# Kernel optimization log

Hardware: AMD Instinct MI355X
Metric: run time of the kernel (lower is better)

The kernel has to match this reference:

```python
import jax, jax.numpy as jnp
import numpy as np

B, S, D = 2, 2048, 1024
H = 16
HD = D // H
SCALE = float(np.sqrt(HD))


def setup_inputs() -> dict:
    key = jax.random.key(0)
    ks = jax.random.split(key, 10)
    def lin(k):
        # xavier_uniform for [out, in] = [D, D]
        bound = float(np.sqrt(6.0 / (D + D)))
        return jax.random.uniform(k, (D, D), jnp.float32, -bound, bound)
    return {
        "hidden_states": jax.random.normal(ks[0], (B, S, D), jnp.float32),
        "attention_mask": jnp.ones((B, S), jnp.float32),
        "Wq": lin(ks[1]), "bq": jnp.zeros((D,), jnp.float32),
        "Wk": lin(ks[2]), "bk": jnp.zeros((D,), jnp.float32),
        "Wv": lin(ks[3]), "bv": jnp.zeros((D,), jnp.float32),
        "Wo": lin(ks[4]), "bo": jnp.zeros((D,), jnp.float32),
    }


def _heads(x):
    # [B,S,D] -> [B,H,S,HD]
    return x.reshape(B, S, H, HD).transpose(0, 2, 1, 3)


def secure_softmax(scores):
    c = jnp.clip(scores, -3.0, 3.0)
    sig = 0.5 + 0.25 * c - 0.01 * c ** 3
    sig = jnp.clip(sig, 0.01, 0.99)
    return sig / (jnp.sum(sig, axis=-1, keepdims=True) + 1e-8)


def reference(hidden_states, attention_mask, Wq, bq, Wk, bk, Wv, bv, Wo, bo):
    q = _heads(hidden_states @ Wq.T + bq)
    k = _heads(hidden_states @ Wk.T + bk)
    v = _heads(hidden_states @ Wv.T + bv)
    # [B,H,S,S]
    scores = jnp.einsum("bhqd,bhkd->bhqk", q, k) / SCALE
    scores = scores + (1.0 - attention_mask[:, None, None, :]) * -10000.0
    probs = secure_softmax(scores)
    ctx = jnp.einsum("bhqk,bhkd->bhqd", probs, v)
    ctx = ctx.transpose(0, 2, 1, 3).reshape(B, S, D)
    return ctx @ Wo.T + bo
```

## Files before the change

### kernel.cpp

```cpp
#include <hip/hip_runtime.h>
#include <stdint.h>

#define B_ 2
#define S_ 2048
#define D_ 1024
#define H_ 16
#define HD_ 64
#define M_ (B_*S_)

typedef __bf16 bf16;
typedef __attribute__((ext_vector_type(8))) __bf16 bf16x8;
typedef __attribute__((ext_vector_type(4))) float f32x4;

__device__ __forceinline__ void gload16(const bf16* g, bf16* l) {
    __builtin_amdgcn_global_load_lds(
        (const __attribute__((address_space(1))) void*)g,
        (__attribute__((address_space(3))) void*)l, 16, 0, 0);
}

__global__ void k_cvt_all(const float* __restrict__ hs,
                          const float* __restrict__ Wq, const float* __restrict__ Wk,
                          const float* __restrict__ Wv, const float* __restrict__ Wo,
                          bf16* __restrict__ hb,
                          bf16* __restrict__ wqb, bf16* __restrict__ wkb,
                          bf16* __restrict__ wvb, bf16* __restrict__ wob) {
    int blk = blockIdx.x;
    const float* s; bf16* d; int base;
    if (blk < 2048) { s = hs; d = hb; base = blk; }
    else {
        int r = blk - 2048; int which = r >> 9; base = r & 511;
        s = (which==0)?Wq:(which==1)?Wk:(which==2)?Wv:Wo;
        d = (which==0)?wqb:(which==1)?wkb:(which==2)?wvb:wob;
    }
    int idx = base*2048 + threadIdx.x*8;
    float4 a = *(const float4*)(s + idx);
    float4 b = *(const float4*)(s + idx + 4);
    bf16 o[8] = {(bf16)a.x,(bf16)a.y,(bf16)a.z,(bf16)a.w,
                 (bf16)b.x,(bf16)b.y,(bf16)b.z,(bf16)b.w};
    *(int4*)(d + idx) = *(const int4*)o;
}

__global__ __launch_bounds__(256) void k_gemm_qkv(
    const bf16* __restrict__ X,
    const bf16* __restrict__ Wq, const bf16* __restrict__ Wk, const bf16* __restrict__ Wv,
    const float* __restrict__ bq, const float* __restrict__ bk, const float* __restrict__ bv,
    bf16* __restrict__ Qo, bf16* __restrict__ Ko, bf16* __restrict__ Vo)
{
    const int z = blockIdx.z;
    const bf16* W = (z==0) ? Wq : (z==1) ? Wk : Wv;
    const float* bias = (z==0) ? bq : (z==1) ? bk : bv;
    const int n0 = blockIdx.x * 128;
    const int m0 = blockIdx.y * 128;
    const int t = threadIdx.x;
    const int w = t >> 6, lane = t & 63, quad = lane >> 4, l15 = lane & 15;
    const int lr = lane >> 3;
    const int lc = (lane & 7) ^ lr;
    const int sx = l15 & 7;
    const int mw = (w >> 1) * 64, nw = (w & 1) * 64;

    __shared__ __align__(16) char smraw[128*136*2];
    bf16* As  = (bf16*)smraw;
    bf16* Bs  = (bf16*)(smraw + 16384);
    bf16* epi = (bf16*)smraw;

    f32x4 acc[4][4];
    #pragma unroll
    for (int i = 0; i < 4; i++)
        #pragma unroll
        for (int j = 0; j < 4; j++)
            acc[i][j] = (f32x4){0.f,0.f,0.f,0.f};

    const bf16* gA = X + (size_t)(m0 + w*8 + lr)*D_ + lc*8;
    const bf16* gB = W + (size_t)(n0 + w*8 + lr)*D_ + lc*8;

    for (int k0 = 0; k0 < D_; k0 += 64) {
        #pragma unroll
        for (int c = 0; c < 4; c++) {
            gload16(gA + (size_t)c*32*D_ + k0, &As[c*2048 + w*512]);
            gload16(gB + (size_t)c*32*D_ + k0, &Bs[c*2048 + w*512]);
        }
        __syncthreads();
        #pragma unroll
        for (int ks = 0; ks < 2; ks++) {
            bf16x8 af[4], bfr[4];
            #pragma unroll
            for (int i = 0; i < 4; i++)
                af[i] = *(const bf16x8*)&As[(mw + i*16 + l15)*64 + (((ks*4+quad)^sx)*8)];
            #pragma unroll
            for (int j = 0; j < 4; j++)
                bfr[j] = *(const bf16x8*)&Bs[(nw + j*16 + l15)*64 + (((ks*4+quad)^sx)*8)];
            #pragma unroll
            for (int i = 0; i < 4; i++)
                #pragma unroll
                for (int j = 0; j < 4; j++)
                    acc[i][j] = __builtin_amdgcn_mfma_f32_16x16x32_bf16(af[i], bfr[j], acc[i][j], 0, 0, 0);
        }
        __syncthreads();
    }

    const float scale = (z == 0) ? 0.125f : 1.0f;
    if (z == 2) {
        #pragma unroll
        for (int j = 0; j < 4; j++) {
            int n = nw + j*16 + l15;
            float bn = bias[n0 + n];
            #pragma unroll
            for (int i = 0; i < 4; i++) {
                int mloc = mw + i*16 + quad*4;
                union { bf16 h4[4]; uint2 u; } pk;
                #pragma unroll
                for (int r = 0; r < 4; r++) pk.h4[r] = (bf16)(acc[i][j][r] + bn);
                *(uint2*)&epi[n*136 + mloc] = pk.u;
            }
        }
    } else {
        #pragma unroll
        for (int j = 0; j < 4; j++) {
            int n = nw + j*16 + l15;
            float bn = bias[n0 + n];
            #pragma unroll
            for (int i = 0; i < 4; i++) {
                int mloc = mw + i*16 + quad*4;
                #pragma unroll
                for (int r = 0; r < 4; r++)
                    epi[(mloc + r)*136 + n] = (bf16)((acc[i][j][r] + bn) * scale);
            }
        }
    }
    __syncthreads();
    if (z == 2) {
        #pragma unroll
        for (int kk = 0; kk < 8; kk++) {
            int c = t + 256*kk;
            int row = c >> 4;
            int mcol = (c & 15) * 8;
            int4 val = *(const int4*)&epi[row*136 + mcol];
            int n = n0 + row; int hh = n >> 6, hd = n & 63;
            int m = m0 + mcol; int bb = m >> 11, s = m & 2047;
            *(int4*)&Vo[((size_t)((bb*H_ + hh)*HD_ + hd))*S_ + s] = val;
        }
    } else {
        bf16* Out = (z == 0) ? Qo : Ko;
        #pragma unroll
        for (int kk = 0; kk < 8; kk++) {
            int c = t + 256*kk;
            int row = c >> 4;
            int ncol = (c & 15) * 8;
            int4 val = *(const int4*)&epi[row*136 + ncol];
            int m = m0 + row; int bb = m >> 11, s = m & 2047;
            int n = n0 + ncol; int hh = n >> 6, hd = n & 63;
            *(int4*)&Out[((size_t)((bb*H_ + hh)*S_ + s))*HD_ + hd] = val;
        }
    }
}

__global__ __launch_bounds__(256) void k_gemm_out(
    const bf16* __restrict__ X, const bf16* __restrict__ W,
    const float* __restrict__ bias, float* __restrict__ Out)
{
    const int n0 = blockIdx.x * 128;
    const int m0 = blockIdx.y * 64;
    const int t = threadIdx.x;
    const int w = t >> 6, lane = t & 63, quad = lane >> 4, l15 = lane & 15;
    const int lr = lane >> 3;
    const int lc = (lane & 7) ^ lr;
    const int sx = l15 & 7;
    const int nw = w * 32;

    __shared__ __align__(16) bf16 As[64*64];
    __shared__ __align__(16) bf16 Bs[128*64];

    f32x4 acc[4][2];
    #pragma unroll
    for (int i = 0; i < 4; i++)
        #pragma unroll
        for (int j = 0; j < 2; j++)
            acc[i][j] = (f32x4){0.f,0.f,0.f,0.f};

    const bf16* gA = X + (size_t)(m0 + w*8 + lr)*D_ + lc*8;
    const bf16* gB = W + (size_t)(n0 + w*8 + lr)*D_ + lc*8;

    for (int k0 = 0; k0 < D_; k0 += 64) {
        #pragma unroll
        for (int c = 0; c < 2; c++)
            gload16(gA + (size_t)c*32*D_ + k0, &As[c*2048 + w*512]);
        #pragma unroll
        for (int c = 0; c < 4; c++)
            gload16(gB + (size_t)c*32*D_ + k0, &Bs[c*2048 + w*512]);
        __syncthreads();
        #pragma unroll
        for (int ks = 0; ks < 2; ks++) {
            bf16x8 af[4], bfr[2];
            #pragma unroll
            for (int i = 0; i < 4; i++)
                af[i] = *(const bf16x8*)&As[(i*16 + l15)*64 + (((ks*4+quad)^sx)*8)];
            #pragma unroll
            for (int j = 0; j < 2; j++)
                bfr[j] = *(const bf16x8*)&Bs[(nw + j*16 + l15)*64 + (((ks*4+quad)^sx)*8)];
            #pragma unroll
            for (int i = 0; i < 4; i++)
                #pragma unroll
                for (int j = 0; j < 2; j++)
                    acc[i][j] = __builtin_amdgcn_mfma_f32_16x16x32_bf16(af[i], bfr[j], acc[i][j], 0, 0, 0);
        }
        __syncthreads();
    }

    #pragma unroll
    for (int j = 0; j < 2; j++) {
        int n = n0 + nw + j*16 + l15;
        float bn = bias[n];
        #pragma unroll
        for (int i = 0; i < 4; i++) {
            int mbase = m0 + i*16 + quad*4;
            #pragma unroll
            for (int r = 0; r < 4; r++)
                Out[(size_t)(mbase + r)*D_ + n] = acc[i][j][r] + bn;
        }
    }
}

__global__ __launch_bounds__(256, 2) void k_attn(
    const bf16* __restrict__ Q, const bf16* __restrict__ K, const bf16* __restrict__ Vt,
    const float* __restrict__ mask, bf16* __restrict__ Ctx)
{
    const int bh = blockIdx.y;
    const int b = bh >> 4, h = bh & 15;
    const int q0 = blockIdx.x * 128;
    const int t = threadIdx.x;
    const int w = t >> 6, lane = t & 63, quad = lane >> 4, l15 = lane & 15;
    const int lr = lane >> 3;
    const int lc = (lane & 7) ^ lr;
    const int sx = l15 & 7;

    __shared__ __align__(16) bf16 Ks[2][64*64];
    __shared__ __align__(16) bf16 Vs[2][64*64];
    __shared__ __align__(16) bf16 Ps[128*64];
    __shared__ float lsumP[4][128];

    bf16x8 qf[8][2];
    const bf16* Qbase = Q + ((size_t)bh*S_ + q0)*HD_;
    #pragma unroll
    for (int qs = 0; qs < 8; qs++)
        #pragma unroll
        for (int ks = 0; ks < 2; ks++)
            qf[qs][ks] = *(const bf16x8*)&Qbase[(size_t)(qs*16 + l15)*HD_ + ks*32 + quad*8];

    f32x4 cacc[2][4];
    #pragma unroll
    for (int i = 0; i < 2; i++)
        #pragma unroll
        for (int j = 0; j < 4; j++)
            cacc[i][j] = (f32x4){0.f,0.f,0.f,0.f};
    float lac[8];
    #pragma unroll
    for (int qs = 0; qs < 8; qs++) lac[qs] = 0.f;

    const bf16* Kst = K + ((size_t)bh*S_ + w*8 + lr)*HD_ + lc*8;
    const bf16* Vst = Vt + ((size_t)bh*HD_ + w*8 + lr)*S_ + lc*8;

    #pragma unroll
    for (int c = 0; c < 2; c++)
        gload16(Kst + (size_t)c*32*HD_, &Ks[0][c*2048 + w*512]);
    #pragma unroll
    for (int c = 0; c < 2; c++)
        gload16(Vst + (size_t)c*32*S_, &Vs[0][c*2048 + w*512]);
    __syncthreads();

    for (int it = 0; it < S_/64; it++) {
        const int cur = it & 1;
        const int k0 = it*64;

        f32x4 st[8];
        #pragma unroll
        for (int qs = 0; qs < 8; qs++) st[qs] = (f32x4){0.f,0.f,0.f,0.f};
        #pragma unroll
        for (int ks = 0; ks < 2; ks++) {
            bf16x8 af = *(const bf16x8*)&Ks[cur][(w*16 + l15)*64 + (((ks*4+quad)^sx)*8)];
            #pragma unroll
            for (int qs = 0; qs < 8; qs++)
                st[qs] = __builtin_amdgcn_mfma_f32_16x16x32_bf16(af, qf[qs][ks], st[qs], 0, 0, 0);
        }

        float4 m4 = *(const float4*)&mask[(size_t)b*S_ + k0 + w*16 + quad*4];
        float mv[4] = {(1.0f-m4.x)*-10000.0f, (1.0f-m4.y)*-10000.0f,
                       (1.0f-m4.z)*-10000.0f, (1.0f-m4.w)*-10000.0f};
        const int c8 = (w*2 + (quad>>1)) ^ sx;
        #pragma unroll
        for (int qs = 0; qs < 8; qs++) {
            union { bf16 h4[4]; uint2 u; } pk;
            #pragma unroll
            for (int r = 0; r < 4; r++) {
                float s = st[qs][r] + mv[r];
                float c = __builtin_amdgcn_fmed3f(s, -3.0f, 3.0f);
                float u = fmaf(c*c, -0.01f, 0.25f);
                float sg = fmaf(c, u, 0.5f);
                sg = __builtin_amdgcn_fmed3f(sg, 0.01f, 0.99f);
                lac[qs] += sg;
                pk.h4[r] = (bf16)sg;
            }
            *(uint2*)&Ps[(qs*16 + l15)*64 + c8*8 + (quad&1)*4] = pk.u;
        }
        __syncthreads();

        if (it < S_/64 - 1) {
            const int nxt = cur ^ 1, k1 = k0 + 64;
            #pragma unroll
            for (int c = 0; c < 2; c++)
                gload16(Kst + (size_t)(k1 + c*32)*HD_, &Ks[nxt][c*2048 + w*512]);
            #pragma unroll
            for (int c = 0; c < 2; c++)
                gload16(Vst + (size_t)c*32*S_ + k1, &Vs[nxt][c*2048 + w*512]);
        }

        #pragma unroll
        for (int ks = 0; ks < 2; ks++) {
            bf16x8 pf[2], vf[4];
            #pragma unroll
            for (int m2 = 0; m2 < 2; m2++)
                pf[m2] = *(const bf16x8*)&Ps[(w*32 + m2*16 + l15)*64 + (((ks*4+quad)^sx)*8)];
            #pragma unroll
            for (int nt = 0; nt < 4; nt++)
                vf[nt] = *(const bf16x8*)&Vs[cur][(nt*16 + l15)*64 + (((ks*4+quad)^sx)*8)];
            #pragma unroll
            for (int m2 = 0; m2 < 2; m2++)
                #pragma unroll
                for (int nt = 0; nt < 4; nt++)
                    cacc[m2][nt] = __builtin_amdgcn_mfma_f32_16x16x32_bf16(pf[m2], vf[nt], cacc[m2][nt], 0, 0, 0);
        }
        __syncthreads();
    }

    #pragma unroll
    for (int qs = 0; qs < 8; qs++) {
        float v = lac[qs];
        v += __shfl_xor(v, 16);
        v += __shfl_xor(v, 32);
        if (quad == 0) lsumP[w][qs*16 + l15] = v;
    }
    __syncthreads();

    #pragma unroll
    for (int m2 = 0; m2 < 2; m2++) {
        #pragma unroll
        for (int r = 0; r < 4; r++) {
            int q = w*32 + m2*16 + quad*4 + r;
            float s = lsumP[0][q] + lsumP[1][q] + lsumP[2][q] + lsumP[3][q];
            float rinv = 1.0f / (s + 1e-8f);
            size_t row = (size_t)(b*S_ + q0 + q);
            #pragma unroll
            for (int nt = 0; nt < 4; nt++)
                Ctx[row*D_ + h*HD_ + nt*16 + l15] = (bf16)(cacc[m2][nt][r] * rinv);
        }
    }
}

extern "C" void kernel_launch(void* const* d_in, const int* in_sizes, int n_in,
                              void* d_out, int out_size, void* d_ws, size_t ws_size,
                              hipStream_t stream) {
    const float* hs   = (const float*)d_in[0];
    const float* mask = (const float*)d_in[1];
    const float* Wq   = (const float*)d_in[2];
    const float* bq   = (const float*)d_in[3];
    const float* Wk   = (const float*)d_in[4];
    const float* bk   = (const float*)d_in[5];
    const float* Wv   = (const float*)d_in[6];
    const float* bv   = (const float*)d_in[7];
    const float* Wo   = (const float*)d_in[8];
    const float* bo   = (const float*)d_in[9];
    float* out = (float*)d_out;

    char* ws = (char*)d_ws;
    const size_t MB = 1024*1024;
    bf16* hb   = (bf16*)(ws);
    bf16* wqb  = (bf16*)(ws + 8*MB);
    bf16* wkb  = (bf16*)(ws + 10*MB);
    bf16* wvb  = (bf16*)(ws + 12*MB);
    bf16* wob  = (bf16*)(ws + 14*MB);
    bf16* qb   = (bf16*)(ws + 16*MB);
    bf16* kb   = (bf16*)(ws + 24*MB);
    bf16* vtb  = (bf16*)(ws + 32*MB);
    bf16* ctxb = (bf16*)(ws + 40*MB);

    k_cvt_all<<<2048 + 4*512, 256, 0, stream>>>(hs, Wq, Wk, Wv, Wo, hb, wqb, wkb, wvb, wob);

    k_gemm_qkv<<<dim3(D_/128, M_/128, 3), 256, 0, stream>>>(
        hb, wqb, wkb, wvb, bq, bk, bv, qb, kb, vtb);

    k_attn<<<dim3(S_/128, B_*H_), 256, 0, stream>>>(qb, kb, vtb, mask, ctxb);

    k_gemm_out<<<dim3(D_/128, M_/64), 256, 0, stream>>>(ctxb, wob, bo, out);
}
```

Measured before the change: 210.4 us.

## Prefetch K and mask earlier, fold mask into MFMA init, pack sigmoid math

```diff
diff --git a/kernel.cpp b/kernel.cpp
--- a/kernel.cpp
+++ b/kernel.cpp
@@ -11,6 +11,7 @@
 typedef __bf16 bf16;
 typedef __attribute__((ext_vector_type(8))) __bf16 bf16x8;
 typedef __attribute__((ext_vector_type(4))) float f32x4;
+typedef __attribute__((ext_vector_type(2))) float f32x2;
 
 __device__ __forceinline__ void gload16(const bf16* g, bf16* l) {
     __builtin_amdgcn_global_load_lds(
@@ -252,12 +253,13 @@
         #pragma unroll
         for (int j = 0; j < 4; j++)
             cacc[i][j] = (f32x4){0.f,0.f,0.f,0.f};
-    float lac[8];
-    #pragma unroll
-    for (int qs = 0; qs < 8; qs++) lac[qs] = 0.f;
+    f32x2 lacv[8];
+    #pragma unroll
+    for (int qs = 0; qs < 8; qs++) lacv[qs] = (f32x2){0.f,0.f};
 
     const bf16* Kst = K + ((size_t)bh*S_ + w*8 + lr)*HD_ + lc*8;
     const bf16* Vst = Vt + ((size_t)bh*HD_ + w*8 + lr)*S_ + lc*8;
+    const float* mrow = mask + (size_t)b*S_ + w*16 + quad*4;
 
     #pragma unroll
     for (int c = 0; c < 2; c++)
@@ -265,49 +267,64 @@
     #pragma unroll
     for (int c = 0; c < 2; c++)
         gload16(Vst + (size_t)c*32*S_, &Vs[0][c*2048 + w*512]);
+    float4 m4 = *(const float4*)&mrow[0];
     __syncthreads();
 
     for (int it = 0; it < S_/64; it++) {
         const int cur = it & 1;
         const int k0 = it*64;
+        const int notlast = (it < S_/64 - 1);
+        const int nxt = cur ^ 1, k1 = k0 + 64;
+
+        float4 m4n;
+        if (notlast) {
+            #pragma unroll
+            for (int c = 0; c < 2; c++)
+                gload16(Kst + (size_t)(k1 + c*32)*HD_, &Ks[nxt][c*2048 + w*512]);
+            m4n = *(const float4*)&mrow[k1];
+        }
+
+        f32x2 mv01 = (f32x2){m4.x, m4.y} * 10000.f - 10000.f;
+        f32x2 mv23 = (f32x2){m4.z, m4.w} * 10000.f - 10000.f;
+        const f32x4 stinit = {mv01.x, mv01.y, mv23.x, mv23.y};
 
         f32x4 st[8];
         #pragma unroll
-        for (int qs = 0; qs < 8; qs++) st[qs] = (f32x4){0.f,0.f,0.f,0.f};
+        for (int qs = 0; qs < 8; qs++) st[qs] = stinit;
         #pragma unroll
         for (int ks = 0; ks < 2; ks++) {
             bf16x8 af = *(const bf16x8*)&Ks[cur][(w*16 + l15)*64 + (((ks*4+quad)^sx)*8)];
+            __builtin_amdgcn_s_setprio(1);
             #pragma unroll
             for (int qs = 0; qs < 8; qs++)
                 st[qs] = __builtin_amdgcn_mfma_f32_16x16x32_bf16(af, qf[qs][ks], st[qs], 0, 0, 0);
-        }
-
-        float4 m4 = *(const float4*)&mask[(size_t)b*S_ + k0 + w*16 + quad*4];
-        float mv[4] = {(1.0f-m4.x)*-10000.0f, (1.0f-m4.y)*-10000.0f,
-                       (1.0f-m4.z)*-10000.0f, (1.0f-m4.w)*-10000.0f};
+            __builtin_amdgcn_s_setprio(0);
+        }
+
+        const f32x2 vn3 = {-3.f, -3.f}, vp3 = {3.f, 3.f};
         const int c8 = (w*2 + (quad>>1)) ^ sx;
         #pragma unroll
         for (int qs = 0; qs < 8; qs++) {
+            f32x2 lo = {st[qs][0], st[qs][1]};
+            f32x2 hi = {st[qs][2], st[qs][3]};
+            lo = __builtin_elementwise_min(__builtin_elementwise_max(lo, vn3), vp3);
+            hi = __builtin_elementwise_min(__builtin_elementwise_max(hi, vn3), vp3);
+            f32x2 ulo = lo * lo;
+            f32x2 uhi = hi * hi;
+            f32x2 tlo = ulo * (-0.01f) + 0.25f;
+            f32x2 thi = uhi * (-0.01f) + 0.25f;
+            f32x2 slo = lo * tlo + 0.5f;
+            f32x2 shi = hi * thi + 0.5f;
+            lacv[qs] += slo;
+            lacv[qs] += shi;
             union { bf16 h4[4]; uint2 u; } pk;
-            #pragma unroll
-            for (int r = 0; r < 4; r++) {
-                float s = st[qs][r] + mv[r];
-                float c = __builtin_amdgcn_fmed3f(s, -3.0f, 3.0f);
-                float u = fmaf(c*c, -0.01f, 0.25f);
-                float sg = fmaf(c, u, 0.5f);
-                sg = __builtin_amdgcn_fmed3f(sg, 0.01f, 0.99f);
-                lac[qs] += sg;
-                pk.h4[r] = (bf16)sg;
-            }
+            pk.h4[0] = (bf16)slo.x; pk.h4[1] = (bf16)slo.y;
+            pk.h4[2] = (bf16)shi.x; pk.h4[3] = (bf16)shi.y;
             *(uint2*)&Ps[(qs*16 + l15)*64 + c8*8 + (quad&1)*4] = pk.u;
         }
         __syncthreads();
 
-        if (it < S_/64 - 1) {
-            const int nxt = cur ^ 1, k1 = k0 + 64;
-            #pragma unroll
-            for (int c = 0; c < 2; c++)
-                gload16(Kst + (size_t)(k1 + c*32)*HD_, &Ks[nxt][c*2048 + w*512]);
+        if (notlast) {
             #pragma unroll
             for (int c = 0; c < 2; c++)
                 gload16(Vst + (size_t)c*32*S_ + k1, &Vs[nxt][c*2048 + w*512]);
@@ -322,18 +339,22 @@
             #pragma unroll
             for (int nt = 0; nt < 4; nt++)
                 vf[nt] = *(const bf16x8*)&Vs[cur][(nt*16 + l15)*64 + (((ks*4+quad)^sx)*8)];
+            __builtin_amdgcn_s_setprio(1);
             #pragma unroll
             for (int m2 = 0; m2 < 2; m2++)
                 #pragma unroll
                 for (int nt = 0; nt < 4; nt++)
                     cacc[m2][nt] = __builtin_amdgcn_mfma_f32_16x16x32_bf16(pf[m2], vf[nt], cacc[m2][nt], 0, 0, 0);
-        }
-        __syncthreads();
+            __builtin_amdgcn_s_setprio(0);
+        }
+        __syncthreads();
+
+        m4 = m4n;
     }
 
     #pragma unroll
     for (int qs = 0; qs < 8; qs++) {
-        float v = lac[qs];
+        float v = lacv[qs].x + lacv[qs].y;
         v += __shfl_xor(v, 16);
         v += __shfl_xor(v, 32);
         if (quad == 0) lsumP[w][qs*16 + l15] = v;
```

Result: no change. 210.7 us (+0.1%).
